# Kernel tuning notes

Measured on AMD Instinct MI355X. Metric: run time of the kernel, lower is better.

The kernel has to match this reference:

```python
import jax, jax.numpy as jnp
import numpy as np

N = 10000
E = 640000
C = 128   # in_channels
H = 512   # hidden_dim
O = 128   # out_channels


def setup_inputs() -> dict:
    key = jax.random.key(0)
    k1, k2, k3, k4, k5, k6, k7 = jax.random.split(key, 7)
    x = jax.random.normal(k1, (N, C), dtype=jnp.float32)
    edge_index = jax.random.randint(k2, (2, E), 0, N, dtype=jnp.int64)
    # MLP params (Linear(2C, H) -> ReLU -> Linear(H, O)), torch default init scale
    w1 = jax.random.uniform(k3, (2 * C, H), jnp.float32, -1, 1) / np.sqrt(2 * C)
    b1 = jax.random.uniform(k4, (H,), jnp.float32, -1, 1) / np.sqrt(2 * C)
    w2 = jax.random.uniform(k5, (H, O), jnp.float32, -1, 1) / np.sqrt(H)
    b2 = jax.random.uniform(k6, (O,), jnp.float32, -1, 1) / np.sqrt(H)
    return {"x": x, "edge_index": edge_index, "w1": w1, "b1": b1, "w2": w2, "b2": b2}


def reference(x, edge_index, w1, b1, w2, b2):
    row, col = edge_index[0], edge_index[1]
    # scatter_mean: mean of source features x[col] into destination row
    summed = jax.ops.segment_sum(x[col], row, num_segments=N)          # [N, C]
    count = jax.ops.segment_sum(jnp.ones((E,), x.dtype), row, num_segments=N)
    neighbor_mean = summed / jnp.maximum(count, 1.0)[:, None]          # [N, C]
    h = jnp.concatenate([x, neighbor_mean], axis=1)                    # [N, 2C]
    h = jax.nn.relu(h @ w1 + b1)                                       # [N, H]
    return h @ w2 + b2                                                 # [N, O]
```

## Files before the change

kernel.cpp:

```cpp
#include <hip/hip_runtime.h>

#define C_IN 128
#define H_DIM 512
#define O_DIM 128
#define CAP   128
#define BM    32
#define FB    16
#define FBT   1024
#define HCAP  10240

typedef __attribute__((ext_vector_type(8))) short short8;
typedef __attribute__((ext_vector_type(4))) float f32x4;

__device__ inline unsigned short f2bf(float f) {
    unsigned int u = __float_as_uint(f);
    unsigned int r = (u + 0x7FFF + ((u >> 16) & 1)) >> 16;
    return (unsigned short)r;
}
__device__ inline float bf2f(unsigned short s) {
    return __uint_as_float(((unsigned int)s) << 16);
}

union SMem {
    float tile[32][33];
    int   hist[HCAP];
};

__global__ __launch_bounds__(FBT)
void prep_fill(const float* __restrict__ w1, unsigned short* __restrict__ w1t,
               const float* __restrict__ w2, unsigned short* __restrict__ w2t,
               const float* __restrict__ x, unsigned short* __restrict__ h0,
               const int* __restrict__ ei, int* __restrict__ cnt,
               unsigned short* __restrict__ bucket, int N, int E) {
    __shared__ SMem sm;
    const int bid = blockIdx.x;
    const int t = threadIdx.x;

    if (bid < FB) {
        const int epb = (E + FB - 1) / FB;
        const int e0 = bid * epb;
        const int e1 = min(E, e0 + epb);
        if (N <= HCAP) {
            for (int r = t; r < N; r += FBT) sm.hist[r] = 0;
            __syncthreads();
            for (int k = e0 + t; k < e1; k += FBT)
                atomicAdd(&sm.hist[ei[k]], 1);
            __syncthreads();
            for (int r = t; r < N; r += FBT) {
                int c = sm.hist[r];
                if (c > 0) sm.hist[r] = atomicAdd(&cnt[r], c);
            }
            __syncthreads();
            for (int k = e0 + t; k < e1; k += FBT) {
                int row = ei[k];
                int col = ei[E + k];
                int slot = atomicAdd(&sm.hist[row], 1);
                if (slot < CAP) bucket[(long)row * CAP + slot] = (unsigned short)col;
            }
        } else {
            for (int k = e0 + t; k < e1; k += FBT) {
                int row = ei[k];
                int col = ei[E + k];
                int slot = atomicAdd(&cnt[row], 1);
                if (slot < CAP) bucket[(long)row * CAP + slot] = (unsigned short)col;
            }
        }
    } else {
        const int pb = bid - FB;
        if (pb < 192) {
            const int tx = t & 31, ty = t >> 5;
            const float* src; unsigned short* dst; int R, Ccols, bx, by;
            if (pb < 128) { src = w1; dst = w1t; R = 2 * C_IN; Ccols = H_DIM; bx = pb & 15; by = pb >> 4; }
            else { int j = pb - 128; src = w2; dst = w2t; R = H_DIM; Ccols = O_DIM; bx = j & 3; by = j >> 2; }
            const int c0 = bx * 32, r0 = by * 32;
            sm.tile[ty][tx] = src[(long)(r0 + ty) * Ccols + c0 + tx];
            __syncthreads();
            dst[(long)(c0 + ty) * R + r0 + tx] = f2bf(sm.tile[tx][ty]);
        }
        const int nb = gridDim.x - FB;
        const int XJ = N * C_IN / 4;
        for (int j = pb * FBT + t; j < XJ; j += nb * FBT) {
            int n = j >> 5, c4 = j & 31;
            float4 v = ((const float4*)x)[j];
            ushort4 s;
            s.x = f2bf(v.x); s.y = f2bf(v.y); s.z = f2bf(v.z); s.w = f2bf(v.w);
            *(ushort4*)(h0 + (long)n * (2 * C_IN) + c4 * 4) = s;
        }
    }
}

__global__ __launch_bounds__(256)
void gather_kernel(const unsigned short* __restrict__ bucket,
                   const int* __restrict__ cnt, unsigned short* __restrict__ h0,
                   int N) {
    const int lane = threadIdx.x & 63;
    const int n = blockIdx.x * 4 + (threadIdx.x >> 6);
    if (n >= N) return;
    const int g = lane >> 4;
    const int l16 = lane & 15;
    const int degt = cnt[n];
    const int deg = min(degt, CAP);

    const unsigned int bb = ((const unsigned int*)bucket)[(long)n * (CAP / 2) + lane];

    float acc[8] = {};
    int e = 0;
    for (; e + 32 <= deg; e += 32) {
        int c[8];
#pragma unroll
        for (int i = 0; i < 8; i++) {
            int k = e + 4 * i + g;
            c[i] = (__shfl(bb, k >> 1) >> ((k & 1) << 4)) & 0xffff;
        }
        short8 u[8];
#pragma unroll
        for (int i = 0; i < 8; i++)
            u[i] = *(const short8*)(h0 + (long)c[i] * (2 * C_IN) + l16 * 8);
#pragma unroll
        for (int j = 0; j < 8; j++) {
            float s0 = bf2f((unsigned short)u[0][j]) + bf2f((unsigned short)u[1][j]);
            float s1 = bf2f((unsigned short)u[2][j]) + bf2f((unsigned short)u[3][j]);
            float s2 = bf2f((unsigned short)u[4][j]) + bf2f((unsigned short)u[5][j]);
            float s3 = bf2f((unsigned short)u[6][j]) + bf2f((unsigned short)u[7][j]);
            acc[j] += (s0 + s1) + (s2 + s3);
        }
    }
    if (e + 16 <= deg) {
        int k0 = e + g, k1 = e + 4 + g, k2 = e + 8 + g, k3 = e + 12 + g;
        int c0 = (__shfl(bb, k0 >> 1) >> ((k0 & 1) << 4)) & 0xffff;
        int c1 = (__shfl(bb, k1 >> 1) >> ((k1 & 1) << 4)) & 0xffff;
        int c2 = (__shfl(bb, k2 >> 1) >> ((k2 & 1) << 4)) & 0xffff;
        int c3 = (__shfl(bb, k3 >> 1) >> ((k3 & 1) << 4)) & 0xffff;
        short8 u0 = *(const short8*)(h0 + (long)c0 * (2 * C_IN) + l16 * 8);
        short8 u1 = *(const short8*)(h0 + (long)c1 * (2 * C_IN) + l16 * 8);
        short8 u2 = *(const short8*)(h0 + (long)c2 * (2 * C_IN) + l16 * 8);
        short8 u3 = *(const short8*)(h0 + (long)c3 * (2 * C_IN) + l16 * 8);
#pragma unroll
        for (int j = 0; j < 8; j++)
            acc[j] += (bf2f((unsigned short)u0[j]) + bf2f((unsigned short)u1[j]))
                    + (bf2f((unsigned short)u2[j]) + bf2f((unsigned short)u3[j]));
        e += 16;
    }
    if (e + 8 <= deg) {
        int k0 = e + g, k1 = e + 4 + g;
        int c0 = (__shfl(bb, k0 >> 1) >> ((k0 & 1) << 4)) & 0xffff;
        int c1 = (__shfl(bb, k1 >> 1) >> ((k1 & 1) << 4)) & 0xffff;
        short8 u0 = *(const short8*)(h0 + (long)c0 * (2 * C_IN) + l16 * 8);
        short8 u1 = *(const short8*)(h0 + (long)c1 * (2 * C_IN) + l16 * 8);
#pragma unroll
        for (int j = 0; j < 8; j++)
            acc[j] += bf2f((unsigned short)u0[j]) + bf2f((unsigned short)u1[j]);
        e += 8;
    }
    if (e + 4 <= deg) {
        int k = e + g;
        int c = (__shfl(bb, k >> 1) >> ((k & 1) << 4)) & 0xffff;
        short8 u = *(const short8*)(h0 + (long)c * (2 * C_IN) + l16 * 8);
#pragma unroll
        for (int j = 0; j < 8; j++) acc[j] += bf2f((unsigned short)u[j]);
        e += 4;
    }
    {
        int rem = deg - e;
        int k = e + g;
        unsigned int bv = __shfl(bb, k >> 1);
        if (g < rem) {
            int c = (bv >> ((k & 1) << 4)) & 0xffff;
            short8 u = *(const short8*)(h0 + (long)c * (2 * C_IN) + l16 * 8);
#pragma unroll
            for (int j = 0; j < 8; j++) acc[j] += bf2f((unsigned short)u[j]);
        }
    }
#pragma unroll
    for (int j = 0; j < 8; j++) {
        acc[j] += __shfl_xor(acc[j], 16, 64);
        acc[j] += __shfl_xor(acc[j], 32, 64);
    }
    if (lane < 16) {
        float inv = 1.0f / fmaxf((float)degt, 1.0f);
        short8 mv;
#pragma unroll
        for (int j = 0; j < 8; j++) mv[j] = (short)f2bf(acc[j] * inv);
        *(short8*)(h0 + (long)n * (2 * C_IN) + C_IN + l16 * 8) = mv;
    }
}

__global__ __launch_bounds__(256)
void fused_mlp(const unsigned short* __restrict__ h0,
               const unsigned short* __restrict__ w1t,
               const float* __restrict__ bias1,
               const unsigned short* __restrict__ w2t,
               const float* __restrict__ bias2,
               float* __restrict__ out, int M) {
    __shared__ __align__(16) unsigned short h1s[BM][520];

    const int t = threadIdx.x;
    const int m0 = blockIdx.x * BM;
    const int lane = t & 63;
    const int w = t >> 6;
    const int l16 = lane & 15;
    const int q = lane >> 4;
    const int q8 = q * 8;

    short8 a_reg[2][8];
#pragma unroll
    for (int mf = 0; mf < 2; mf++) {
        int gm = m0 + mf * 16 + l16;
        if (gm < M) {
            const unsigned short* ap = h0 + (long)gm * (2 * C_IN) + q8;
#pragma unroll
            for (int s = 0; s < 8; s++) a_reg[mf][s] = *(const short8*)(ap + s * 32);
        } else {
#pragma unroll
            for (int s = 0; s < 8; s++) a_reg[mf][s] = short8{};
        }
    }

#pragma unroll
    for (int nc = 0; nc < 4; nc++) {
        const int colbase = w * 128 + nc * 32;
        f32x4 acc[2][2] = {};
#pragma unroll
        for (int s = 0; s < 8; s++) {
            short8 b0 = *(const short8*)(w1t + (long)(colbase + l16) * 256 + s * 32 + q8);
            short8 b1 = *(const short8*)(w1t + (long)(colbase + 16 + l16) * 256 + s * 32 + q8);
            acc[0][0] = __builtin_amdgcn_mfma_f32_16x16x32_bf16(a_reg[0][s], b0, acc[0][0], 0, 0, 0);
            acc[0][1] = __builtin_amdgcn_mfma_f32_16x16x32_bf16(a_reg[0][s], b1, acc[0][1], 0, 0, 0);
            acc[1][0] = __builtin_amdgcn_mfma_f32_16x16x32_bf16(a_reg[1][s], b0, acc[1][0], 0, 0, 0);
            acc[1][1] = __builtin_amdgcn_mfma_f32_16x16x32_bf16(a_reg[1][s], b1, acc[1][1], 0, 0, 0);
        }
        float bb0 = bias1[colbase + l16];
        float bb1 = bias1[colbase + 16 + l16];
#pragma unroll
        for (int mf = 0; mf < 2; mf++) {
#pragma unroll
            for (int r = 0; r < 4; r++) {
                int m = mf * 16 + q * 4 + r;
                h1s[m][colbase + l16]      = f2bf(fmaxf(acc[mf][0][r] + bb0, 0.f));
                h1s[m][colbase + 16 + l16] = f2bf(fmaxf(acc[mf][1][r] + bb1, 0.f));
            }
        }
    }
    __syncthreads();

    f32x4 acc2[2][2] = {};
    const int wn = w * 32;
#pragma unroll
    for (int ks = 0; ks < 16; ks++) {
        short8 a0 = *(const short8*)&h1s[l16][ks * 32 + q8];
        short8 a1 = *(const short8*)&h1s[16 + l16][ks * 32 + q8];
        short8 b0 = *(const short8*)(w2t + (long)(wn + l16) * H_DIM + ks * 32 + q8);
        short8 b1 = *(const short8*)(w2t + (long)(wn + 16 + l16) * H_DIM + ks * 32 + q8);
        acc2[0][0] = __builtin_amdgcn_mfma_f32_16x16x32_bf16(a0, b0, acc2[0][0], 0, 0, 0);
        acc2[0][1] = __builtin_amdgcn_mfma_f32_16x16x32_bf16(a0, b1, acc2[0][1], 0, 0, 0);
        acc2[1][0] = __builtin_amdgcn_mfma_f32_16x16x32_bf16(a1, b0, acc2[1][0], 0, 0, 0);
        acc2[1][1] = __builtin_amdgcn_mfma_f32_16x16x32_bf16(a1, b1, acc2[1][1], 0, 0, 0);
    }
#pragma unroll
    for (int mf = 0; mf < 2; mf++) {
#pragma unroll
        for (int nf = 0; nf < 2; nf++) {
            int gn = wn + nf * 16 + l16;
            float bb = bias2[gn];
#pragma unroll
            for (int r = 0; r < 4; r++) {
                int gm = m0 + mf * 16 + q * 4 + r;
                if (gm < M) out[(long)gm * O_DIM + gn] = acc2[mf][nf][r] + bb;
            }
        }
    }
}

extern "C" void kernel_launch(void* const* d_in, const int* in_sizes, int n_in,
                              void* d_out, int out_size, void* d_ws, size_t ws_size,
                              hipStream_t stream) {
    const float* x  = (const float*)d_in[0];
    const int*   ei = (const int*)d_in[1];
    const float* w1 = (const float*)d_in[2];
    const float* b1 = (const float*)d_in[3];
    const float* w2 = (const float*)d_in[4];
    const float* b2 = (const float*)d_in[5];
    float* out = (float*)d_out;

    const int N = in_sizes[0] / C_IN;
    const int E = in_sizes[1] / 2;

    unsigned short* h0b = (unsigned short*)d_ws;
    unsigned short* w1t = h0b + (size_t)N * (2 * C_IN);
    unsigned short* w2t = w1t + (size_t)H_DIM * (2 * C_IN);
    int* cnt = (int*)(w2t + (size_t)O_DIM * H_DIM);
    unsigned short* bucket = (unsigned short*)(cnt + (size_t)N);

    hipMemsetAsync(cnt, 0, (size_t)N * sizeof(int), stream);
    prep_fill<<<FB + 240, FBT, 0, stream>>>(w1, w1t, w2, w2t, x, h0b, ei, cnt, bucket, N, E);
    gather_kernel<<<(N + 3) / 4, 256, 0, stream>>>(bucket, cnt, h0b, N);
    fused_mlp<<<(N + BM - 1) / BM, 256, 0, stream>>>(h0b, w1t, b1, w2t, b2, out, N);
}
```

Before: 166.2 us.

## Split CSR bucket fill into per-block histogram, prefix scan, and scatter kernels

The old single kernel, 16 blocks of 1024 threads, built the histogram and then did global atomics on cnt before scattering. It is replaced by three kernels: 64 blocks write per-block histograms to a workspace array, a prefix kernel computes each block's per-row offsets and the total counts, and a scatter kernel fills buckets using shared-memory cursors. This removes the global atomics and the memset and spreads edge processing over more blocks. The cost is two extra launches and 64*N ints of extra workspace traffic, and the prep blocks shrink to 256 threads with a looped weight transpose.

```diff
diff --git a/kernel.cpp b/kernel.cpp
--- a/kernel.cpp
+++ b/kernel.cpp
@@ -5,8 +5,7 @@
 #define O_DIM 128
 #define CAP   128
 #define BM    32
-#define FB    16
-#define FBT   1024
+#define FBLK  64
 #define HCAP  10240
 
 typedef __attribute__((ext_vector_type(8))) short short8;
@@ -26,65 +25,98 @@
     int   hist[HCAP];
 };
 
-__global__ __launch_bounds__(FBT)
-void prep_fill(const float* __restrict__ w1, unsigned short* __restrict__ w1t,
+__global__ __launch_bounds__(256)
+void hist_prep(const float* __restrict__ w1, unsigned short* __restrict__ w1t,
                const float* __restrict__ w2, unsigned short* __restrict__ w2t,
                const float* __restrict__ x, unsigned short* __restrict__ h0,
-               const int* __restrict__ ei, int* __restrict__ cnt,
-               unsigned short* __restrict__ bucket, int N, int E) {
+               const int* __restrict__ ei, int* __restrict__ cnt_blk,
+               int N, int E) {
     __shared__ SMem sm;
     const int bid = blockIdx.x;
     const int t = threadIdx.x;
 
-    if (bid < FB) {
-        const int epb = (E + FB - 1) / FB;
+    if (bid < FBLK) {
+        const int epb = (E + FBLK - 1) / FBLK;
         const int e0 = bid * epb;
         const int e1 = min(E, e0 + epb);
         if (N <= HCAP) {
-            for (int r = t; r < N; r += FBT) sm.hist[r] = 0;
+            for (int r = t; r < N; r += 256) sm.hist[r] = 0;
             __syncthreads();
-            for (int k = e0 + t; k < e1; k += FBT)
+            for (int k = e0 + t; k < e1; k += 256)
                 atomicAdd(&sm.hist[ei[k]], 1);
             __syncthreads();
-            for (int r = t; r < N; r += FBT) {
-                int c = sm.hist[r];
-                if (c > 0) sm.hist[r] = atomicAdd(&cnt[r], c);
-            }
+            for (int r = t; r < N; r += 256) cnt_blk[bid * N + r] = sm.hist[r];
+        } else {
+            for (int r = t; r < N; r += 256) cnt_blk[bid * N + r] = 0;
             __syncthreads();
-            for (int k = e0 + t; k < e1; k += FBT) {
-                int row = ei[k];
-                int col = ei[E + k];
-                int slot = atomicAdd(&sm.hist[row], 1);
-                if (slot < CAP) bucket[(long)row * CAP + slot] = (unsigned short)col;
-            }
-        } else {
-            for (int k = e0 + t; k < e1; k += FBT) {
-                int row = ei[k];
-                int col = ei[E + k];
-                int slot = atomicAdd(&cnt[row], 1);
-                if (slot < CAP) bucket[(long)row * CAP + slot] = (unsigned short)col;
-            }
+            for (int k = e0 + t; k < e1; k += 256)
+                atomicAdd(&cnt_blk[bid * N + ei[k]], 1);
         }
     } else {
-        const int pb = bid - FB;
+        const int pb = bid - FBLK;
         if (pb < 192) {
-            const int tx = t & 31, ty = t >> 5;
             const float* src; unsigned short* dst; int R, Ccols, bx, by;
             if (pb < 128) { src = w1; dst = w1t; R = 2 * C_IN; Ccols = H_DIM; bx = pb & 15; by = pb >> 4; }
             else { int j = pb - 128; src = w2; dst = w2t; R = H_DIM; Ccols = O_DIM; bx = j & 3; by = j >> 2; }
             const int c0 = bx * 32, r0 = by * 32;
-            sm.tile[ty][tx] = src[(long)(r0 + ty) * Ccols + c0 + tx];
+            const int tx = t & 31, ty = t >> 5;
+#pragma unroll
+            for (int i = 0; i < 32; i += 8)
+                sm.tile[ty + i][tx] = src[(long)(r0 + ty + i) * Ccols + c0 + tx];
             __syncthreads();
-            dst[(long)(c0 + ty) * R + r0 + tx] = f2bf(sm.tile[tx][ty]);
-        }
-        const int nb = gridDim.x - FB;
+#pragma unroll
+            for (int i = 0; i < 32; i += 8)
+                dst[(long)(c0 + ty + i) * R + r0 + tx] = f2bf(sm.tile[tx][ty + i]);
+        }
         const int XJ = N * C_IN / 4;
-        for (int j = pb * FBT + t; j < XJ; j += nb * FBT) {
+        for (int j = pb * 256 + t; j < XJ; j += 256 * 256) {
             int n = j >> 5, c4 = j & 31;
             float4 v = ((const float4*)x)[j];
             ushort4 s;
             s.x = f2bf(v.x); s.y = f2bf(v.y); s.z = f2bf(v.z); s.w = f2bf(v.w);
             *(ushort4*)(h0 + (long)n * (2 * C_IN) + c4 * 4) = s;
+        }
+    }
+}
+
+__global__ __launch_bounds__(256)
+void prefix_kernel(int* __restrict__ cnt_blk, int* __restrict__ cnt, int N) {
+    int r = blockIdx.x * 256 + threadIdx.x;
+    if (r >= N) return;
+    int run = 0;
+#pragma unroll 8
+    for (int b = 0; b < FBLK; b++) {
+        int c = cnt_blk[b * N + r];
+        cnt_blk[b * N + r] = run;
+        run += c;
+    }
+    cnt[r] = run;
+}
+
+__global__ __launch_bounds__(256)
+void scatter_kernel(const int* __restrict__ ei, int* __restrict__ cnt_blk,
+                    unsigned short* __restrict__ bucket, int N, int E) {
+    __shared__ int cur[HCAP];
+    const int bid = blockIdx.x;
+    const int t = threadIdx.x;
+    const int epb = (E + FBLK - 1) / FBLK;
+    const int e0 = bid * epb;
+    const int e1 = min(E, e0 + epb);
+    if (N <= HCAP) {
+        for (int r = t; r < N; r += 256) cur[r] = cnt_blk[bid * N + r];
+        __syncthreads();
+        for (int k = e0 + t; k < e1; k += 256) {
+            int row = ei[k];
+            int col = ei[E + k];
+            int slot = atomicAdd(&cur[row], 1);
+            if (slot < CAP) bucket[(long)row * CAP + slot] = (unsigned short)col;
+        }
+    } else {
+        for (int k = e0 + t; k < e1; k += 256) {
+            int row = ei[k];
+            int col = ei[E + k];
+            int slot = atomicAdd(&cnt_blk[bid * N + row], 1);
+            if (slot < CAP) bucket[(long)row * CAP + slot] = (unsigned short)col;
         }
     }
 }
@@ -289,10 +321,12 @@
     unsigned short* w1t = h0b + (size_t)N * (2 * C_IN);
     unsigned short* w2t = w1t + (size_t)H_DIM * (2 * C_IN);
     int* cnt = (int*)(w2t + (size_t)O_DIM * H_DIM);
-    unsigned short* bucket = (unsigned short*)(cnt + (size_t)N);
-
-    hipMemsetAsync(cnt, 0, (size_t)N * sizeof(int), stream);
-    prep_fill<<<FB + 240, FBT, 0, stream>>>(w1, w1t, w2, w2t, x, h0b, ei, cnt, bucket, N, E);
+    int* cnt_blk = cnt + (size_t)N;
+    unsigned short* bucket = (unsigned short*)(cnt_blk + (size_t)FBLK * N);
+
+    hist_prep<<<FBLK + 256, 256, 0, stream>>>(w1, w1t, w2, w2t, x, h0b, ei, cnt_blk, N, E);
+    prefix_kernel<<<(N + 255) / 256, 256, 0, stream>>>(cnt_blk, cnt, N);
+    scatter_kernel<<<FBLK, 256, 0, stream>>>(ei, cnt_blk, bucket, N, E);
     gather_kernel<<<(N + 3) / 4, 256, 0, stream>>>(bucket, cnt, h0b, N);
     fused_mlp<<<(N + BM - 1) / BM, 256, 0, stream>>>(h0b, w1t, b1, w2t, b2, out, N);
 }
```

After: 159.1 us. 1.04x faster.

## Partition bucket fill by row range with shared-memory counters, drop global atomics

Applied to the files above, without the earlier changes.

The bucket fill now gives each of 64 blocks a contiguous range of destination rows. Each block scans the whole edge list with int4 loads, keeps edges whose row falls in its range, and takes slots from shared-memory counters. It then writes cnt directly, which removes the global atomics and the memset. The bf16 x and mean features move into two separate buffers, so the MLP reads its A operand from both. The cost is that every fill block reads the full row array, 64 times more index traffic than before, and the bucket layout becomes deterministic per block.

```diff
diff --git a/kernel.cpp b/kernel.cpp
--- a/kernel.cpp
+++ b/kernel.cpp
@@ -5,9 +5,8 @@
 #define O_DIM 128
 #define CAP   128
 #define BM    32
-#define FB    16
-#define FBT   1024
-#define HCAP  10240
+#define FILLB 64
+#define RPB   160
 
 typedef __attribute__((ext_vector_type(8))) short short8;
 typedef __attribute__((ext_vector_type(4))) float f32x4;
@@ -21,78 +20,75 @@
     return __uint_as_float(((unsigned int)s) << 16);
 }
 
-union SMem {
-    float tile[32][33];
-    int   hist[HCAP];
-};
-
-__global__ __launch_bounds__(FBT)
+__global__ __launch_bounds__(1024)
 void prep_fill(const float* __restrict__ w1, unsigned short* __restrict__ w1t,
                const float* __restrict__ w2, unsigned short* __restrict__ w2t,
-               const float* __restrict__ x, unsigned short* __restrict__ h0,
+               const float* __restrict__ x, unsigned short* __restrict__ xb,
                const int* __restrict__ ei, int* __restrict__ cnt,
                unsigned short* __restrict__ bucket, int N, int E) {
-    __shared__ SMem sm;
+    __shared__ int cur[RPB];
+    __shared__ float tile[32][33];
     const int bid = blockIdx.x;
     const int t = threadIdx.x;
 
-    if (bid < FB) {
-        const int epb = (E + FB - 1) / FB;
-        const int e0 = bid * epb;
-        const int e1 = min(E, e0 + epb);
-        if (N <= HCAP) {
-            for (int r = t; r < N; r += FBT) sm.hist[r] = 0;
-            __syncthreads();
-            for (int k = e0 + t; k < e1; k += FBT)
-                atomicAdd(&sm.hist[ei[k]], 1);
-            __syncthreads();
-            for (int r = t; r < N; r += FBT) {
-                int c = sm.hist[r];
-                if (c > 0) sm.hist[r] = atomicAdd(&cnt[r], c);
-            }
-            __syncthreads();
-            for (int k = e0 + t; k < e1; k += FBT) {
-                int row = ei[k];
+    if (bid < FILLB) {
+        const int rpb = (N + FILLB - 1) / FILLB;
+        const int r0 = bid * rpb;
+        const int r1 = min(N, r0 + rpb);
+        for (int r = t; r < rpb; r += 1024) cur[r] = 0;
+        __syncthreads();
+
+        const int E4 = E >> 2;
+        for (int k4 = t; k4 < E4; k4 += 1024) {
+            int4 rr = ((const int4*)ei)[k4];
+#pragma unroll
+            for (int i = 0; i < 4; i++) {
+                int row = (i == 0) ? rr.x : (i == 1) ? rr.y : (i == 2) ? rr.z : rr.w;
+                if (row >= r0 && row < r1) {
+                    int col = ei[E + k4 * 4 + i];
+                    int slot = atomicAdd(&cur[row - r0], 1);
+                    if (slot < CAP) bucket[(long)row * CAP + slot] = (unsigned short)col;
+                }
+            }
+        }
+        for (int k = E4 * 4 + t; k < E; k += 1024) {
+            int row = ei[k];
+            if (row >= r0 && row < r1) {
                 int col = ei[E + k];
-                int slot = atomicAdd(&sm.hist[row], 1);
+                int slot = atomicAdd(&cur[row - r0], 1);
                 if (slot < CAP) bucket[(long)row * CAP + slot] = (unsigned short)col;
             }
-        } else {
-            for (int k = e0 + t; k < e1; k += FBT) {
-                int row = ei[k];
-                int col = ei[E + k];
-                int slot = atomicAdd(&cnt[row], 1);
-                if (slot < CAP) bucket[(long)row * CAP + slot] = (unsigned short)col;
-            }
-        }
+        }
+        __syncthreads();
+        for (int r = r0 + t; r < r1; r += 1024) cnt[r] = cur[r - r0];
     } else {
-        const int pb = bid - FB;
+        const int pb = bid - FILLB;
         if (pb < 192) {
-            const int tx = t & 31, ty = t >> 5;
             const float* src; unsigned short* dst; int R, Ccols, bx, by;
             if (pb < 128) { src = w1; dst = w1t; R = 2 * C_IN; Ccols = H_DIM; bx = pb & 15; by = pb >> 4; }
             else { int j = pb - 128; src = w2; dst = w2t; R = H_DIM; Ccols = O_DIM; bx = j & 3; by = j >> 2; }
             const int c0 = bx * 32, r0 = by * 32;
-            sm.tile[ty][tx] = src[(long)(r0 + ty) * Ccols + c0 + tx];
+            const int tx = t & 31, ty = t >> 5;
+            tile[ty][tx] = src[(long)(r0 + ty) * Ccols + c0 + tx];
             __syncthreads();
-            dst[(long)(c0 + ty) * R + r0 + tx] = f2bf(sm.tile[tx][ty]);
-        }
-        const int nb = gridDim.x - FB;
+            dst[(long)(c0 + ty) * R + r0 + tx] = f2bf(tile[tx][ty]);
+        }
         const int XJ = N * C_IN / 4;
-        for (int j = pb * FBT + t; j < XJ; j += nb * FBT) {
+        for (int j = pb * 1024 + t; j < XJ; j += 256 * 1024) {
             int n = j >> 5, c4 = j & 31;
             float4 v = ((const float4*)x)[j];
             ushort4 s;
             s.x = f2bf(v.x); s.y = f2bf(v.y); s.z = f2bf(v.z); s.w = f2bf(v.w);
-            *(ushort4*)(h0 + (long)n * (2 * C_IN) + c4 * 4) = s;
+            *(ushort4*)(xb + (long)n * C_IN + c4 * 4) = s;
         }
     }
 }
 
 __global__ __launch_bounds__(256)
 void gather_kernel(const unsigned short* __restrict__ bucket,
-                   const int* __restrict__ cnt, unsigned short* __restrict__ h0,
-                   int N) {
+                   const int* __restrict__ cnt,
+                   const unsigned short* __restrict__ xb,
+                   unsigned short* __restrict__ meanb, int N) {
     const int lane = threadIdx.x & 63;
     const int n = blockIdx.x * 4 + (threadIdx.x >> 6);
     if (n >= N) return;
@@ -115,7 +111,7 @@
         short8 u[8];
 #pragma unroll
         for (int i = 0; i < 8; i++)
-            u[i] = *(const short8*)(h0 + (long)c[i] * (2 * C_IN) + l16 * 8);
+            u[i] = *(const short8*)(xb + (long)c[i] * C_IN + l16 * 8);
 #pragma unroll
         for (int j = 0; j < 8; j++) {
             float s0 = bf2f((unsigned short)u[0][j]) + bf2f((unsigned short)u[1][j]);
@@ -131,10 +127,10 @@
         int c1 = (__shfl(bb, k1 >> 1) >> ((k1 & 1) << 4)) & 0xffff;
         int c2 = (__shfl(bb, k2 >> 1) >> ((k2 & 1) << 4)) & 0xffff;
         int c3 = (__shfl(bb, k3 >> 1) >> ((k3 & 1) << 4)) & 0xffff;
-        short8 u0 = *(const short8*)(h0 + (long)c0 * (2 * C_IN) + l16 * 8);
-        short8 u1 = *(const short8*)(h0 + (long)c1 * (2 * C_IN) + l16 * 8);
-        short8 u2 = *(const short8*)(h0 + (long)c2 * (2 * C_IN) + l16 * 8);
-        short8 u3 = *(const short8*)(h0 + (long)c3 * (2 * C_IN) + l16 * 8);
+        short8 u0 = *(const short8*)(xb + (long)c0 * C_IN + l16 * 8);
+        short8 u1 = *(const short8*)(xb + (long)c1 * C_IN + l16 * 8);
+        short8 u2 = *(const short8*)(xb + (long)c2 * C_IN + l16 * 8);
+        short8 u3 = *(const short8*)(xb + (long)c3 * C_IN + l16 * 8);
 #pragma unroll
         for (int j = 0; j < 8; j++)
             acc[j] += (bf2f((unsigned short)u0[j]) + bf2f((unsigned short)u1[j]))
@@ -145,8 +141,8 @@
         int k0 = e + g, k1 = e + 4 + g;
         int c0 = (__shfl(bb, k0 >> 1) >> ((k0 & 1) << 4)) & 0xffff;
         int c1 = (__shfl(bb, k1 >> 1) >> ((k1 & 1) << 4)) & 0xffff;
-        short8 u0 = *(const short8*)(h0 + (long)c0 * (2 * C_IN) + l16 * 8);
-        short8 u1 = *(const short8*)(h0 + (long)c1 * (2 * C_IN) + l16 * 8);
+        short8 u0 = *(const short8*)(xb + (long)c0 * C_IN + l16 * 8);
+        short8 u1 = *(const short8*)(xb + (long)c1 * C_IN + l16 * 8);
 #pragma unroll
         for (int j = 0; j < 8; j++)
             acc[j] += bf2f((unsigned short)u0[j]) + bf2f((unsigned short)u1[j]);
@@ -155,7 +151,7 @@
     if (e + 4 <= deg) {
         int k = e + g;
         int c = (__shfl(bb, k >> 1) >> ((k & 1) << 4)) & 0xffff;
-        short8 u = *(const short8*)(h0 + (long)c * (2 * C_IN) + l16 * 8);
+        short8 u = *(const short8*)(xb + (long)c * C_IN + l16 * 8);
 #pragma unroll
         for (int j = 0; j < 8; j++) acc[j] += bf2f((unsigned short)u[j]);
         e += 4;
@@ -166,7 +162,7 @@
         unsigned int bv = __shfl(bb, k >> 1);
         if (g < rem) {
             int c = (bv >> ((k & 1) << 4)) & 0xffff;
-            short8 u = *(const short8*)(h0 + (long)c * (2 * C_IN) + l16 * 8);
+            short8 u = *(const short8*)(xb + (long)c * C_IN + l16 * 8);
 #pragma unroll
             for (int j = 0; j < 8; j++) acc[j] += bf2f((unsigned short)u[j]);
         }
@@ -181,12 +177,13 @@
         short8 mv;
 #pragma unroll
         for (int j = 0; j < 8; j++) mv[j] = (short)f2bf(acc[j] * inv);
-        *(short8*)(h0 + (long)n * (2 * C_IN) + C_IN + l16 * 8) = mv;
+        *(short8*)(meanb + (long)n * C_IN + l16 * 8) = mv;
     }
 }
 
 __global__ __launch_bounds__(256)
-void fused_mlp(const unsigned short* __restrict__ h0,
+void fused_mlp(const unsigned short* __restrict__ xb,
+               const unsigned short* __restrict__ meanb,
                const unsigned short* __restrict__ w1t,
                const float* __restrict__ bias1,
                const unsigned short* __restrict__ w2t,
@@ -207,9 +204,13 @@
     for (int mf = 0; mf < 2; mf++) {
         int gm = m0 + mf * 16 + l16;
         if (gm < M) {
-            const unsigned short* ap = h0 + (long)gm * (2 * C_IN) + q8;
-#pragma unroll
-            for (int s = 0; s < 8; s++) a_reg[mf][s] = *(const short8*)(ap + s * 32);
+            const unsigned short* ap = xb + (long)gm * C_IN + q8;
+            const unsigned short* mp = meanb + (long)gm * C_IN + q8;
+#pragma unroll
+            for (int s = 0; s < 4; s++) {
+                a_reg[mf][s]     = *(const short8*)(ap + s * 32);
+                a_reg[mf][4 + s] = *(const short8*)(mp + s * 32);
+            }
         } else {
 #pragma unroll
             for (int s = 0; s < 8; s++) a_reg[mf][s] = short8{};
@@ -285,14 +286,14 @@
     const int N = in_sizes[0] / C_IN;
     const int E = in_sizes[1] / 2;
 
-    unsigned short* h0b = (unsigned short*)d_ws;
-    unsigned short* w1t = h0b + (size_t)N * (2 * C_IN);
+    unsigned short* xb = (unsigned short*)d_ws;
+    unsigned short* meanb = xb + (size_t)N * C_IN;
+    unsigned short* w1t = meanb + (size_t)N * C_IN;
     unsigned short* w2t = w1t + (size_t)H_DIM * (2 * C_IN);
     int* cnt = (int*)(w2t + (size_t)O_DIM * H_DIM);
     unsigned short* bucket = (unsigned short*)(cnt + (size_t)N);
 
-    hipMemsetAsync(cnt, 0, (size_t)N * sizeof(int), stream);
-    prep_fill<<<FB + 240, FBT, 0, stream>>>(w1, w1t, w2, w2t, x, h0b, ei, cnt, bucket, N, E);
-    gather_kernel<<<(N + 3) / 4, 256, 0, stream>>>(bucket, cnt, h0b, N);
-    fused_mlp<<<(N + BM - 1) / BM, 256, 0, stream>>>(h0b, w1t, b1, w2t, b2, out, N);
-}
+    prep_fill<<<FILLB + 256, 1024, 0, stream>>>(w1, w1t, w2, w2t, x, xb, ei, cnt, bucket, N, E);
+    gather_kernel<<<(N + 3) / 4, 256, 0, stream>>>(bucket, cnt, xb, meanb, N);
+    fused_mlp<<<(N + BM - 1) / BM, 256, 0, stream>>>(xb, meanb, w1t, b1, w2t, b2, out, N);
+}
```

After: 278.9 us. 1.68x slower.
